# Optimization experiments

Measured on AMD Instinct MI355X. Metric: run time of the kernel, lower is better.

Reference implementation:

```python
import jax, jax.numpy as jnp
import numpy as np

LEAKY_RELU_SLOPE = 0.2
N = 8192
F = 256


def setup_inputs() -> dict:
    key = jax.random.key(0)
    k1, k2, k3 = jax.random.split(key, 3)
    h = jax.random.normal(k1, (N, F), dtype=jnp.float32)
    # sparse-ish adjacency with guaranteed self-loops so no row is all -inf
    adjacency = jax.random.bernoulli(k2, 0.05, (N, N))
    adjacency = adjacency.at[jnp.arange(N), jnp.arange(N)].set(True)
    # xavier_uniform for a: shape (F, 2), gain=1 -> limit = sqrt(6/(F+2))
    limit = float(np.sqrt(6.0 / (F + 2)))
    a = jax.random.uniform(k3, (F, 2), minval=-limit, maxval=limit, dtype=jnp.float32)
    return {"h": h, "adjacency": adjacency, "a": a}


def reference(h, adjacency, a):
    e = h @ a                      # [N, 2]
    e1 = e[:, 0:1]                 # [N, 1]
    e2 = e[:, 1:2]                 # [N, 1]
    scores = e1 + e2.T             # [N, N] broadcast
    scores = jnp.where(scores >= 0, scores, LEAKY_RELU_SLOPE * scores)
    scores = jnp.where(adjacency, scores, -jnp.inf)
    return jax.nn.softmax(scores, axis=1)
```

## Files before the change

kernel.cpp:

```cpp
#include <hip/hip_runtime.h>

#define GN 8192
#define GF 256
#define SLOPE 0.2f

__global__ void detect_mode_kernel(const unsigned int* __restrict__ adj,
                                   int* __restrict__ mode) {
    __shared__ int s_byte, s_float;
    if (threadIdx.x == 0) { s_byte = 0; s_float = 0; }
    __syncthreads();
    int any_byte = 0, any_float = 0;
    for (int i = threadIdx.x; i < 16384; i += 256) {
        unsigned int w = adj[i];
        if (w == 0x3F800000u) any_float = 1;
        else if (w > 1u && (w & 0xFEFEFEFEu) == 0u) any_byte = 1;
    }
    if (any_byte)  atomicOr(&s_byte, 1);
    if (any_float) atomicOr(&s_float, 1);
    __syncthreads();
    if (threadIdx.x == 0) *mode = s_byte ? 1 : (s_float ? 2 : 0);
}

__global__ __launch_bounds__(256) void compute_e_kernel(
        const float* __restrict__ h, const float* __restrict__ a,
        float* __restrict__ e1, float* __restrict__ e2) {
    int wave = threadIdx.x >> 6;
    int lane = threadIdx.x & 63;
    int row  = blockIdx.x * 4 + wave;

    const float4* h4 = (const float4*)(h + (size_t)row * GF);
    float4 hv = h4[lane];
    const float4* a4 = (const float4*)a;
    float4 av0 = a4[2 * lane];
    float4 av1 = a4[2 * lane + 1];

    float d1 = hv.x * av0.x + hv.y * av0.z + hv.z * av1.x + hv.w * av1.z;
    float d2 = hv.x * av0.y + hv.y * av0.w + hv.z * av1.y + hv.w * av1.w;
    #pragma unroll
    for (int off = 32; off; off >>= 1) {
        d1 += __shfl_xor(d1, off);
        d2 += __shfl_xor(d2, off);
    }
    if (lane == 0) {
        e1[row] = d1;
        e2[row] = d2;
    }
}

template <int MODE>
__device__ __forceinline__ void attn_row_body(
        const void* __restrict__ adjv,
        const float* __restrict__ e1, const float* __restrict__ e2,
        float* __restrict__ out) {
    const int row = blockIdx.x;
    const int tid = threadIdx.x;
    const float se1 = e1[row];
    const size_t rowbase = (size_t)row * GN;
    const size_t vecbase = rowbase >> 2;

    const float4* e2v = (const float4*)e2;

    float v[32];
    float acc = 0.f;

    #pragma unroll
    for (int c = 0; c < 8; ++c) {
        const int j4 = c * 256 + tid;
        float4 ev = e2v[j4];
        bool m0, m1, m2, m3;
        if (MODE == 0) {
            int4 aw = ((const int4*)adjv)[vecbase + j4];
            m0 = aw.x != 0; m1 = aw.y != 0; m2 = aw.z != 0; m3 = aw.w != 0;
        } else if (MODE == 1) {
            unsigned int aw = ((const unsigned int*)adjv)[vecbase + j4];
            m0 = (aw & 0x000000FFu) != 0; m1 = (aw & 0x0000FF00u) != 0;
            m2 = (aw & 0x00FF0000u) != 0; m3 = (aw & 0xFF000000u) != 0;
        } else {
            float4 aw = ((const float4*)adjv)[vecbase + j4];
            m0 = aw.x != 0.f; m1 = aw.y != 0.f; m2 = aw.z != 0.f; m3 = aw.w != 0.f;
        }
        float s0 = se1 + ev.x; s0 = s0 >= 0.f ? s0 : SLOPE * s0;
        float s1 = se1 + ev.y; s1 = s1 >= 0.f ? s1 : SLOPE * s1;
        float s2 = se1 + ev.z; s2 = s2 >= 0.f ? s2 : SLOPE * s2;
        float s3 = se1 + ev.w; s3 = s3 >= 0.f ? s3 : SLOPE * s3;
        float x0 = m0 ? __expf(s0) : 0.f;
        float x1 = m1 ? __expf(s1) : 0.f;
        float x2 = m2 ? __expf(s2) : 0.f;
        float x3 = m3 ? __expf(s3) : 0.f;
        v[c * 4 + 0] = x0; v[c * 4 + 1] = x1;
        v[c * 4 + 2] = x2; v[c * 4 + 3] = x3;
        acc += x0 + x1 + x2 + x3;
    }

    #pragma unroll
    for (int off = 32; off; off >>= 1) acc += __shfl_xor(acc, off);
    __shared__ float wsum[4];
    if ((tid & 63) == 0) wsum[tid >> 6] = acc;
    __syncthreads();
    const float total = wsum[0] + wsum[1] + wsum[2] + wsum[3];
    const float inv = 1.0f / total;

    float4* out4 = (float4*)(out + rowbase);
    #pragma unroll
    for (int c = 0; c < 8; ++c) {
        float4 o;
        o.x = v[c * 4 + 0] * inv; o.y = v[c * 4 + 1] * inv;
        o.z = v[c * 4 + 2] * inv; o.w = v[c * 4 + 3] * inv;
        out4[c * 256 + tid] = o;
    }
}

__global__ __launch_bounds__(256) void attn_row_kernel(
        const int* __restrict__ mode, const void* __restrict__ adjv,
        const float* __restrict__ e1, const float* __restrict__ e2,
        float* __restrict__ out) {
    const int m = *mode;
    if (m == 0)      attn_row_body<0>(adjv, e1, e2, out);
    else if (m == 1) attn_row_body<1>(adjv, e1, e2, out);
    else             attn_row_body<2>(adjv, e1, e2, out);
}

extern "C" void kernel_launch(void* const* d_in, const int* in_sizes, int n_in,
                              void* d_out, int out_size, void* d_ws, size_t ws_size,
                              hipStream_t stream) {
    const float* h   = (const float*)d_in[0];
    const void*  adj = (const void*)d_in[1];
    const float* a   = (const float*)d_in[2];
    float* out = (float*)d_out;

    int*   mode = (int*)d_ws;
    float* e1   = (float*)((char*)d_ws + 256);
    float* e2   = e1 + GN;

    detect_mode_kernel<<<1, 256, 0, stream>>>((const unsigned int*)adj, mode);
    compute_e_kernel<<<GN / 4, 256, 0, stream>>>(h, a, e1, e2);
    attn_row_kernel<<<GN, 256, 0, stream>>>(mode, adj, e1, e2, out);
}
```

Measured before the change: 473.8 us.

## Fuse adjacency-mode detection into row kernel, use 512 threads and nontemporal I/O

Removes the separate single-block mode-detection launch; each row block now inspects the first 8 KB of the adjacency itself and picks the decode path locally. The row kernel is widened to 512 threads with 16 values per thread, and the adjacency loads and output stores become nontemporal so streaming data does not pollute cache. This saves one launch and its serialization but adds a redundant small read per block, and detection now looks at fewer words than before.

```diff
diff --git a/kernel.cpp b/kernel.cpp
--- a/kernel.cpp
+++ b/kernel.cpp
@@ -4,22 +4,8 @@
 #define GF 256
 #define SLOPE 0.2f
 
-__global__ void detect_mode_kernel(const unsigned int* __restrict__ adj,
-                                   int* __restrict__ mode) {
-    __shared__ int s_byte, s_float;
-    if (threadIdx.x == 0) { s_byte = 0; s_float = 0; }
-    __syncthreads();
-    int any_byte = 0, any_float = 0;
-    for (int i = threadIdx.x; i < 16384; i += 256) {
-        unsigned int w = adj[i];
-        if (w == 0x3F800000u) any_float = 1;
-        else if (w > 1u && (w & 0xFEFEFEFEu) == 0u) any_byte = 1;
-    }
-    if (any_byte)  atomicOr(&s_byte, 1);
-    if (any_float) atomicOr(&s_float, 1);
-    __syncthreads();
-    if (threadIdx.x == 0) *mode = s_byte ? 1 : (s_float ? 2 : 0);
-}
+typedef int   vint4   __attribute__((ext_vector_type(4)));
+typedef float vfloat4 __attribute__((ext_vector_type(4)));
 
 __global__ __launch_bounds__(256) void compute_e_kernel(
         const float* __restrict__ h, const float* __restrict__ a,
@@ -51,32 +37,32 @@
 __device__ __forceinline__ void attn_row_body(
         const void* __restrict__ adjv,
         const float* __restrict__ e1, const float* __restrict__ e2,
-        float* __restrict__ out) {
+        float* __restrict__ out, float* __restrict__ wsum) {
     const int row = blockIdx.x;
     const int tid = threadIdx.x;
     const float se1 = e1[row];
     const size_t rowbase = (size_t)row * GN;
-    const size_t vecbase = rowbase >> 2;
+    const size_t vecbase = (size_t)row * 2048;
 
     const float4* e2v = (const float4*)e2;
 
-    float v[32];
+    float v[16];
     float acc = 0.f;
 
     #pragma unroll
-    for (int c = 0; c < 8; ++c) {
-        const int j4 = c * 256 + tid;
+    for (int c = 0; c < 4; ++c) {
+        const int j4 = c * 512 + tid;
         float4 ev = e2v[j4];
         bool m0, m1, m2, m3;
         if (MODE == 0) {
-            int4 aw = ((const int4*)adjv)[vecbase + j4];
+            vint4 aw = __builtin_nontemporal_load(&((const vint4*)adjv)[vecbase + j4]);
             m0 = aw.x != 0; m1 = aw.y != 0; m2 = aw.z != 0; m3 = aw.w != 0;
         } else if (MODE == 1) {
-            unsigned int aw = ((const unsigned int*)adjv)[vecbase + j4];
+            unsigned int aw = __builtin_nontemporal_load(&((const unsigned int*)adjv)[vecbase + j4]);
             m0 = (aw & 0x000000FFu) != 0; m1 = (aw & 0x0000FF00u) != 0;
             m2 = (aw & 0x00FF0000u) != 0; m3 = (aw & 0xFF000000u) != 0;
         } else {
-            float4 aw = ((const float4*)adjv)[vecbase + j4];
+            vfloat4 aw = __builtin_nontemporal_load(&((const vfloat4*)adjv)[vecbase + j4]);
             m0 = aw.x != 0.f; m1 = aw.y != 0.f; m2 = aw.z != 0.f; m3 = aw.w != 0.f;
         }
         float s0 = se1 + ev.x; s0 = s0 >= 0.f ? s0 : SLOPE * s0;
@@ -94,30 +80,49 @@
 
     #pragma unroll
     for (int off = 32; off; off >>= 1) acc += __shfl_xor(acc, off);
-    __shared__ float wsum[4];
     if ((tid & 63) == 0) wsum[tid >> 6] = acc;
     __syncthreads();
-    const float total = wsum[0] + wsum[1] + wsum[2] + wsum[3];
+    float total = 0.f;
+    #pragma unroll
+    for (int w = 0; w < 8; ++w) total += wsum[w];
     const float inv = 1.0f / total;
 
-    float4* out4 = (float4*)(out + rowbase);
+    vfloat4* out4 = (vfloat4*)(out + rowbase);
     #pragma unroll
-    for (int c = 0; c < 8; ++c) {
-        float4 o;
+    for (int c = 0; c < 4; ++c) {
+        vfloat4 o;
         o.x = v[c * 4 + 0] * inv; o.y = v[c * 4 + 1] * inv;
         o.z = v[c * 4 + 2] * inv; o.w = v[c * 4 + 3] * inv;
-        out4[c * 256 + tid] = o;
+        __builtin_nontemporal_store(o, &out4[c * 512 + tid]);
     }
 }
 
-__global__ __launch_bounds__(256) void attn_row_kernel(
-        const int* __restrict__ mode, const void* __restrict__ adjv,
+__global__ __launch_bounds__(512) void attn_row_kernel(
+        const void* __restrict__ adjv,
         const float* __restrict__ e1, const float* __restrict__ e2,
         float* __restrict__ out) {
-    const int m = *mode;
-    if (m == 0)      attn_row_body<0>(adjv, e1, e2, out);
-    else if (m == 1) attn_row_body<1>(adjv, e1, e2, out);
-    else             attn_row_body<2>(adjv, e1, e2, out);
+    __shared__ int s_flags;
+    __shared__ float wsum[8];
+    const int tid = threadIdx.x;
+    if (tid == 0) s_flags = 0;
+    __syncthreads();
+
+    uint4 hw = ((const uint4*)adjv)[tid];
+    int f = 0;
+    {
+        unsigned int w;
+        w = hw.x; if (w == 0x3F800000u) f |= 2; else if (w > 1u && (w & 0xFEFEFEFEu) == 0u) f |= 1;
+        w = hw.y; if (w == 0x3F800000u) f |= 2; else if (w > 1u && (w & 0xFEFEFEFEu) == 0u) f |= 1;
+        w = hw.z; if (w == 0x3F800000u) f |= 2; else if (w > 1u && (w & 0xFEFEFEFEu) == 0u) f |= 1;
+        w = hw.w; if (w == 0x3F800000u) f |= 2; else if (w > 1u && (w & 0xFEFEFEFEu) == 0u) f |= 1;
+    }
+    if (f) atomicOr(&s_flags, f);
+    __syncthreads();
+    const int mode = (s_flags & 1) ? 1 : ((s_flags & 2) ? 2 : 0);
+
+    if (mode == 0)      attn_row_body<0>(adjv, e1, e2, out, wsum);
+    else if (mode == 1) attn_row_body<1>(adjv, e1, e2, out, wsum);
+    else                attn_row_body<2>(adjv, e1, e2, out, wsum);
 }
 
 extern "C" void kernel_launch(void* const* d_in, const int* in_sizes, int n_in,
@@ -128,11 +133,9 @@
     const float* a   = (const float*)d_in[2];
     float* out = (float*)d_out;
 
-    int*   mode = (int*)d_ws;
-    float* e1   = (float*)((char*)d_ws + 256);
-    float* e2   = e1 + GN;
+    float* e1 = (float*)d_ws;
+    float* e2 = e1 + GN;
 
-    detect_mode_kernel<<<1, 256, 0, stream>>>((const unsigned int*)adj, mode);
     compute_e_kernel<<<GN / 4, 256, 0, stream>>>(h, a, e1, e2);
-    attn_row_kernel<<<GN, 256, 0, stream>>>(mode, adj, e1, e2, out);
+    attn_row_kernel<<<GN, 512, 0, stream>>>(adj, e1, e2, out);
 }
```

Result: faster. 437.7 us (-7.6%).
